# Kernel optimization log

Hardware: AMD Instinct MI355X
Metric: run time of the kernel (lower is better)

Reference implementation:

```python
import jax, jax.numpy as jnp
import numpy as np

B, P = 8, 1024
NUM_BINS = 11


def setup_inputs() -> dict:
    key = jax.random.key(0)
    x = jax.random.normal(key, (B, P, 6), dtype=jnp.float32)
    return {"x": x, "num_bins": NUM_BINS}


def reference(x, num_bins):
    Bv, Pv, _ = x.shape
    eps = 1e-6
    pos = x[..., 0:3]            # [B,P,3]
    ori = x[..., 3:6]            # [B,P,3]

    # axis 1 = i (source point), axis 2 = j (pair point)
    delta = pos[:, None, :, :] - pos[:, :, None, :]          # pj - pi: [B,P,P,3]
    ni = ori[:, :, None, :]                                   # [B,P,1,3]
    nj = ori[:, None, :, :]                                   # [B,1,P,3]

    dist = jnp.sqrt(jnp.sum(delta * delta, axis=-1))          # [B,P,P]

    ni_b = jnp.broadcast_to(ni, delta.shape)
    v = jnp.cross(delta, ni_b, axis=-1)
    v = v / (jnp.linalg.norm(v, axis=-1, keepdims=True) + eps)
    w = jnp.cross(ni_b, v, axis=-1)
    w = w / (jnp.linalg.norm(w, axis=-1, keepdims=True) + eps)

    alpha = jnp.sum(v * nj, axis=-1)                          # [B,P,P]
    phi = jnp.sum(ni * delta, axis=-1) / (dist + eps)         # [B,P,P]
    theta = jnp.arctan2(jnp.sum(w * nj, axis=-1),
                        jnp.sum(ni * nj, axis=-1)) / jnp.pi   # [B,P,P]

    def to_idx(a):
        # map [-1,1] -> bin index, truncation toward zero like torch .to(int64)
        idx = ((a + 1.0) * 0.5 * num_bins).astype(jnp.int32)
        return jnp.minimum(idx, num_bins - 1)

    fpfh_idx = (to_idx(alpha) * num_bins + to_idx(phi)) * num_bins + to_idx(theta)
    fpfh_idx = fpfh_idx.reshape(Bv, Pv * Pv)                  # [B, P*P]

    # exclude diagonal (i == j) pairs via zero weight, equivalent to the
    # eye-masked gather in the original (diagonal entries are finite)
    offdiag = (1.0 - jnp.eye(Pv, dtype=jnp.float32)).reshape(Pv * Pv)
    weights = jnp.broadcast_to(offdiag, (Bv, Pv * Pv))

    num_dim_feat = num_bins * num_bins * num_bins
    freq = jnp.zeros((Bv, num_dim_feat), dtype=jnp.float32)
    freq = freq.at[jnp.arange(Bv)[:, None], fpfh_idx].add(weights)
    freq = freq / (Pv * (Pv - 1))
    return freq
```

## Files before the change

kernel.cpp:

```cpp
#include <hip/hip_runtime.h>

#define P 1024
#define NB 11
#define NBINS 1331
#define BATCH 8
#define TI 8
#define NIT (P / TI)
#define BLKT 512

#define RFL(f) __uint_as_float(__builtin_amdgcn_readfirstlane(__float_as_uint(f)))

__global__ __launch_bounds__(BLKT, 8) void fpfh_main(const float* __restrict__ x,
                                                     int* __restrict__ part,
                                                     int npart) {
    __shared__ int shist[NBINS];

    const int t  = threadIdx.x;
    const int b  = blockIdx.y;
    const int i0 = blockIdx.x * TI;
    const float* xb = x + b * (P * 6);

    for (int z = t; z < NBINS; z += BLKT) shist[z] = 0;

    float PIX[TI], PIY[TI], PIZ[TI], NIX[TI], NIY[TI], NIZ[TI], NII[TI], SNI[TI];
    #pragma unroll
    for (int il = 0; il < TI; ++il) {
        const float* xi = xb + (i0 + il) * 6;
        PIX[il] = RFL(xi[0]); PIY[il] = RFL(xi[1]); PIZ[il] = RFL(xi[2]);
        NIX[il] = RFL(xi[3]); NIY[il] = RFL(xi[4]); NIZ[il] = RFL(xi[5]);
        float nii = fmaf(NIX[il], NIX[il], fmaf(NIY[il], NIY[il], NIZ[il] * NIZ[il]));
        NII[il] = RFL(nii);
        SNI[il] = RFL(__builtin_amdgcn_sqrtf(nii));
    }

    float pjx[2], pjy[2], pjz[2], njx[2], njy[2], njz[2];
    #pragma unroll
    for (int jt = 0; jt < 2; ++jt) {
        const float* xj = xb + (jt * BLKT + t) * 6;
        pjx[jt] = xj[0]; pjy[jt] = xj[1]; pjz[jt] = xj[2];
        njx[jt] = xj[3]; njy[jt] = xj[4]; njz[jt] = xj[5];
    }

    __syncthreads();

    #pragma unroll
    for (int jt = 0; jt < 2; ++jt) {
        const int j = jt * BLKT + t;

        #pragma unroll
        for (int il = 0; il < TI; ++il) {
            const float dx = pjx[jt] - PIX[il];
            const float dy = pjy[jt] - PIY[il];
            const float dz = pjz[jt] - PIZ[il];

            const float dd    = fmaf(dx, dx, fmaf(dy, dy, dz * dz));
            const float nid   = fmaf(NIX[il], dx, fmaf(NIY[il], dy, NIZ[il] * dz));
            const float nidnj = fmaf(NIX[il], njx[jt],
                                fmaf(NIY[il], njy[jt], NIZ[il] * njz[jt]));
            const float ddnj  = fmaf(dx, njx[jt], fmaf(dy, njy[jt], dz * njz[jt]));

            const float cvx = fmaf(dy, NIZ[il], -(dz * NIY[il]));
            const float cvy = fmaf(dz, NIX[il], -(dx * NIZ[il]));
            const float cvz = fmaf(dx, NIY[il], -(dy * NIX[il]));
            const float cvdnj = fmaf(cvx, njx[jt],
                                fmaf(cvy, njy[jt], cvz * njz[jt]));

            float cvv = fmaxf(fmaf(dd, NII[il], -(nid * nid)), 0.0f);
            const float rs    = __builtin_amdgcn_rsqf(cvv);
            const float alpha = cvdnj * rs;
            const float scv   = cvv * rs;

            const float phi = nid * __builtin_amdgcn_rsqf(dd);

            const float y_t = fmaf(NII[il], ddnj, -(nid * nidnj));
            const float x_t = (SNI[il] * nidnj) * scv;
            const float tq  = x_t * __builtin_amdgcn_rcpf(__builtin_fabsf(y_t));
            int kk = (tq <  3.40568625f) + (tq <  0.86650494f) + (tq < 0.14377830f)
                   + (tq < -0.45668469f) + (tq < -1.55603037f);
            const int ith = (y_t < 0.0f) ? 5 - kk : 5 + kk;

            int ia = min((int)fmaf(alpha, 5.5f, 5.5f), NB - 1);
            int ip = min((int)fmaf(phi,   5.5f, 5.5f), NB - 1);

            int bin = (ia * NB + ip) * NB + ith;
            if (bin < 0) bin += NBINS;
            if ((j != i0 + il) && ((unsigned)bin < (unsigned)NBINS))
                atomicAdd(&shist[bin], 1);
        }
    }
    __syncthreads();

    if (npart == NIT) {
        int* slot = part + (b * NIT + blockIdx.x) * NBINS;
        for (int z = t; z < NBINS; z += BLKT) slot[z] = shist[z];
    } else {
        int* slot = part + (b * npart + (blockIdx.x % npart)) * NBINS;
        for (int z = t; z < NBINS; z += BLKT) {
            int c = shist[z];
            if (c) atomicAdd(&slot[z], c);
        }
    }
}

__global__ __launch_bounds__(256) void fpfh_reduce(const int* __restrict__ part,
                                                   float* __restrict__ out,
                                                   int npart) {
    const int tid = blockIdx.x * 256 + threadIdx.x;
    const int o   = tid >> 2;
    const int q   = tid & 3;
    int s = 0;
    if (o < BATCH * NBINS) {
        const int b   = o / NBINS;
        const int bin = o - b * NBINS;
        const int* p  = part + (size_t)b * npart * NBINS + bin;
        for (int k = q; k < npart; k += 4)
            s += p[(size_t)k * NBINS];
    }
    s += __shfl_xor(s, 1);
    s += __shfl_xor(s, 2);
    if (q == 0 && o < BATCH * NBINS)
        out[o] = (float)s * (1.0f / 1047552.0f);
}

extern "C" void kernel_launch(void* const* d_in, const int* in_sizes, int n_in,
                              void* d_out, int out_size, void* d_ws, size_t ws_size,
                              hipStream_t stream) {
    const float* x = (const float*)d_in[0];
    float* out = (float*)d_out;
    int* part  = (int*)d_ws;

    const size_t slot_bytes = (size_t)BATCH * NBINS * sizeof(int);
    const size_t need_excl  = slot_bytes * NIT;
    int npart;
    if (ws_size >= need_excl) {
        npart = NIT;
    } else {
        npart = (int)(ws_size / slot_bytes);
        if (npart < 1)   npart = 1;
        if (npart > NIT) npart = NIT;
        hipMemsetAsync(d_ws, 0, slot_bytes * npart, stream);
    }

    dim3 grid(NIT, BATCH);
    fpfh_main<<<grid, BLKT, 0, stream>>>(x, part, npart);

    const int nThreads = BATCH * NBINS * 4;
    fpfh_reduce<<<(nThreads + 255) / 256, 256, 0, stream>>>(part, out, npart);
}
```

Before: 30.28 us.

## Exploit pair symmetry to compute both (i,j) and (j,i) bins per pair

```diff
diff --git a/kernel.cpp b/kernel.cpp
--- a/kernel.cpp
+++ b/kernel.cpp
@@ -6,21 +6,41 @@
 #define BATCH 8
 #define TI 8
 #define NIT (P / TI)
-#define BLKT 512
 
 #define RFL(f) __uint_as_float(__builtin_amdgcn_readfirstlane(__float_as_uint(f)))
 
-__global__ __launch_bounds__(BLKT, 8) void fpfh_main(const float* __restrict__ x,
-                                                     int* __restrict__ part,
-                                                     int npart) {
+__device__ __forceinline__ int bin_of(float nii, float sni, float ao, float ax,
+                                      float ninj, float t3, float dd, float rdd) {
+    float cvv = fmaxf(fmaf(dd, nii, -(ao * ao)), 0.0f);
+    float rs  = __builtin_amdgcn_rsqf(cvv);
+    float alpha = t3 * rs;
+    float scv = cvv * rs;
+    float phi = ao * rdd;
+    float y   = fmaf(nii, ax, -(ao * ninj));
+    float xx  = (sni * ninj) * scv;
+    float tq  = xx * __builtin_amdgcn_rcpf(__builtin_fabsf(y));
+    int kk = (tq <  3.40568625f) + (tq <  0.86650494f) + (tq < 0.14377830f)
+           + (tq < -0.45668469f) + (tq < -1.55603037f);
+    int ith = (y < 0.0f) ? 5 - kk : 5 + kk;
+    int ia = min((int)fmaf(alpha, 5.5f, 5.5f), NB - 1);
+    int ip = min((int)fmaf(phi,   5.5f, 5.5f), NB - 1);
+    int bin = (ia * NB + ip) * NB + ith;
+    if (bin < 0) bin += NBINS;
+    return bin;
+}
+
+__global__ __launch_bounds__(256, 8) void fpfh_main(const float* __restrict__ x,
+                                                    int* __restrict__ part,
+                                                    int npart) {
     __shared__ int shist[NBINS];
 
     const int t  = threadIdx.x;
+    const int T  = blockIdx.x;
     const int b  = blockIdx.y;
-    const int i0 = blockIdx.x * TI;
+    const int i0 = T * TI;
     const float* xb = x + b * (P * 6);
 
-    for (int z = t; z < NBINS; z += BLKT) shist[z] = 0;
+    for (int z = t; z < NBINS; z += 256) shist[z] = 0;
 
     float PIX[TI], PIY[TI], PIZ[TI], NIX[TI], NIY[TI], NIZ[TI], NII[TI], SNI[TI];
     #pragma unroll
@@ -33,69 +53,80 @@
         SNI[il] = RFL(__builtin_amdgcn_sqrtf(nii));
     }
 
-    float pjx[2], pjy[2], pjz[2], njx[2], njy[2], njz[2];
-    #pragma unroll
-    for (int jt = 0; jt < 2; ++jt) {
-        const float* xj = xb + (jt * BLKT + t) * 6;
-        pjx[jt] = xj[0]; pjy[jt] = xj[1]; pjz[jt] = xj[2];
-        njx[jt] = xj[3]; njy[jt] = xj[4]; njz[jt] = xj[5];
+    const int j0 = (i0 + 8 + t) & (P - 1);
+    const bool uno1 = (t < 248);
+    const int j1 = uno1 ? ((i0 + 264 + t) & (P - 1)) : (i0 + (t - 248));
+    const bool condA = (T < 64) && (t < 8);
+    const int jc = i0 + 512 + t;
+
+    const float* xj0 = xb + j0 * 6;
+    const float p0x = xj0[0], p0y = xj0[1], p0z = xj0[2];
+    const float n0x = xj0[3], n0y = xj0[4], n0z = xj0[5];
+    const float njj0 = fmaf(n0x, n0x, fmaf(n0y, n0y, n0z * n0z));
+    const float snj0 = __builtin_amdgcn_sqrtf(njj0);
+
+    const float* xj1 = xb + j1 * 6;
+    const float p1x = xj1[0], p1y = xj1[1], p1z = xj1[2];
+    const float n1x = xj1[3], n1y = xj1[4], n1z = xj1[5];
+    const float njj1 = fmaf(n1x, n1x, fmaf(n1y, n1y, n1z * n1z));
+    const float snj1 = __builtin_amdgcn_sqrtf(njj1);
+
+    float pcx = 0, pcy = 0, pcz = 0, ncx = 0, ncy = 0, ncz = 0, njjc = 0, snjc = 0;
+    if (condA) {
+        const float* xjc = xb + jc * 6;
+        pcx = xjc[0]; pcy = xjc[1]; pcz = xjc[2];
+        ncx = xjc[3]; ncy = xjc[4]; ncz = xjc[5];
+        njjc = fmaf(ncx, ncx, fmaf(ncy, ncy, ncz * ncz));
+        snjc = __builtin_amdgcn_sqrtf(njjc);
     }
 
     __syncthreads();
 
+#define BODY(JV, PX, PY, PZ, NX, NY, NZ, NJJ, SNJ, UNO)                        \
+    {                                                                          \
+        const float dx = PX - PIX[il];                                         \
+        const float dy = PY - PIY[il];                                         \
+        const float dz = PZ - PIZ[il];                                         \
+        const float dd   = fmaf(dx, dx, fmaf(dy, dy, dz * dz));                \
+        const float nid  = fmaf(NIX[il], dx, fmaf(NIY[il], dy, NIZ[il] * dz)); \
+        const float njd  = fmaf(NX, dx, fmaf(NY, dy, NZ * dz));                \
+        const float ninj = fmaf(NIX[il], NX, fmaf(NIY[il], NY, NIZ[il] * NZ)); \
+        const float cvx  = fmaf(dy, NIZ[il], -(dz * NIY[il]));                 \
+        const float cvy  = fmaf(dz, NIX[il], -(dx * NIZ[il]));                 \
+        const float cvz  = fmaf(dx, NIY[il], -(dy * NIX[il]));                 \
+        const float t3   = fmaf(cvx, NX, fmaf(cvy, NY, cvz * NZ));             \
+        const float rdd  = __builtin_amdgcn_rsqf(dd);                          \
+        const int bin1 = bin_of(NII[il], SNI[il],  nid,  njd, ninj, t3, dd, rdd); \
+        const bool e1 = ((UNO) || (JV) != i0 + il) && ((unsigned)bin1 < (unsigned)NBINS); \
+        if (e1) atomicAdd(&shist[bin1], 1);                                    \
+        if (UNO) {                                                             \
+            const int bin2 = bin_of(NJJ, SNJ, -njd, -nid, ninj, t3, dd, rdd);  \
+            if ((unsigned)bin2 < (unsigned)NBINS) atomicAdd(&shist[bin2], 1);  \
+        }                                                                      \
+    }
+
     #pragma unroll
-    for (int jt = 0; jt < 2; ++jt) {
-        const int j = jt * BLKT + t;
+    for (int il = 0; il < TI; ++il)
+        BODY(j0, p0x, p0y, p0z, n0x, n0y, n0z, njj0, snj0, true)
 
+    #pragma unroll
+    for (int il = 0; il < TI; ++il)
+        BODY(j1, p1x, p1y, p1z, n1x, n1y, n1z, njj1, snj1, uno1)
+
+    if (condA) {
         #pragma unroll
-        for (int il = 0; il < TI; ++il) {
-            const float dx = pjx[jt] - PIX[il];
-            const float dy = pjy[jt] - PIY[il];
-            const float dz = pjz[jt] - PIZ[il];
-
-            const float dd    = fmaf(dx, dx, fmaf(dy, dy, dz * dz));
-            const float nid   = fmaf(NIX[il], dx, fmaf(NIY[il], dy, NIZ[il] * dz));
-            const float nidnj = fmaf(NIX[il], njx[jt],
-                                fmaf(NIY[il], njy[jt], NIZ[il] * njz[jt]));
-            const float ddnj  = fmaf(dx, njx[jt], fmaf(dy, njy[jt], dz * njz[jt]));
-
-            const float cvx = fmaf(dy, NIZ[il], -(dz * NIY[il]));
-            const float cvy = fmaf(dz, NIX[il], -(dx * NIZ[il]));
-            const float cvz = fmaf(dx, NIY[il], -(dy * NIX[il]));
-            const float cvdnj = fmaf(cvx, njx[jt],
-                                fmaf(cvy, njy[jt], cvz * njz[jt]));
-
-            float cvv = fmaxf(fmaf(dd, NII[il], -(nid * nid)), 0.0f);
-            const float rs    = __builtin_amdgcn_rsqf(cvv);
-            const float alpha = cvdnj * rs;
-            const float scv   = cvv * rs;
-
-            const float phi = nid * __builtin_amdgcn_rsqf(dd);
-
-            const float y_t = fmaf(NII[il], ddnj, -(nid * nidnj));
-            const float x_t = (SNI[il] * nidnj) * scv;
-            const float tq  = x_t * __builtin_amdgcn_rcpf(__builtin_fabsf(y_t));
-            int kk = (tq <  3.40568625f) + (tq <  0.86650494f) + (tq < 0.14377830f)
-                   + (tq < -0.45668469f) + (tq < -1.55603037f);
-            const int ith = (y_t < 0.0f) ? 5 - kk : 5 + kk;
-
-            int ia = min((int)fmaf(alpha, 5.5f, 5.5f), NB - 1);
-            int ip = min((int)fmaf(phi,   5.5f, 5.5f), NB - 1);
-
-            int bin = (ia * NB + ip) * NB + ith;
-            if (bin < 0) bin += NBINS;
-            if ((j != i0 + il) && ((unsigned)bin < (unsigned)NBINS))
-                atomicAdd(&shist[bin], 1);
-        }
+        for (int il = 0; il < TI; ++il)
+            BODY(jc, pcx, pcy, pcz, ncx, ncy, ncz, njjc, snjc, true)
     }
+#undef BODY
     __syncthreads();
 
     if (npart == NIT) {
         int* slot = part + (b * NIT + blockIdx.x) * NBINS;
-        for (int z = t; z < NBINS; z += BLKT) slot[z] = shist[z];
+        for (int z = t; z < NBINS; z += 256) slot[z] = shist[z];
     } else {
         int* slot = part + (b * npart + (blockIdx.x % npart)) * NBINS;
-        for (int z = t; z < NBINS; z += BLKT) {
+        for (int z = t; z < NBINS; z += 256) {
             int c = shist[z];
             if (c) atomicAdd(&slot[z], c);
         }
@@ -142,7 +173,7 @@
     }
 
     dim3 grid(NIT, BATCH);
-    fpfh_main<<<grid, BLKT, 0, stream>>>(x, part, npart);
+    fpfh_main<<<grid, 256, 0, stream>>>(x, part, npart);
 
     const int nThreads = BATCH * NBINS * 4;
     fpfh_reduce<<<(nThreads + 255) / 256, 256, 0, stream>>>(part, out, npart);
```

Result: no change. 30.88 us (+2.0%).
